# Performance work log

Hardware: AMD Instinct MI355X
Metric: run time of the kernel (lower is better)

Reference implementation:

```python
import jax, jax.numpy as jnp
import numpy as np

B, N, D, NH, T = 4, 1024, 512, 8, 2
H = D // NH  # attention_head_size = 64
NTYPES = 8


def setup_inputs() -> dict:
    key = jax.random.key(0)
    ks = jax.random.split(key, 16)
    w = lambda k, s: jax.random.normal(k, s, jnp.float32) * 0.05
    inp = {
        'node_embedding': jax.random.normal(ks[0], (B, N, D), jnp.float32),
        'question_embedding': jax.random.normal(ks[1], (B, 1, D), jnp.float32),
        'W_fc_w': w(ks[2], (D, 2 * D)),
        'w_dc_w': w(ks[3], (T, 2 * D, D)),
        'dense_w': w(ks[4], (2 * D, 2 * D)),
        'ln_in_g': jnp.ones((2 * D,), jnp.float32), 'ln_in_b': jnp.zeros((2 * D,), jnp.float32),
        'W_qv_w': w(ks[5], (2 * D, D)), 'W_kv_w': w(ks[6], (2 * D, D)), 'W_vv_w': w(ks[7], (2 * D, D)),
        'W_qc_w': w(ks[8], (D, D)), 'W_kc_w': w(ks[9], (D, D)), 'W_vc_w': w(ks[10], (D, D)),
        'ln_q_g': jnp.ones((D,), jnp.float32), 'ln_q_b': jnp.zeros((D,), jnp.float32),
        'ln_k_g': jnp.ones((D,), jnp.float32), 'ln_k_b': jnp.zeros((D,), jnp.float32),
        'ln_v_g': jnp.ones((D,), jnp.float32), 'ln_v_b': jnp.zeros((D,), jnp.float32),
        'W_att': w(ks[11], (1 + NTYPES, 2 * H)),  # row 0 = entity-number, rows 1..8 = number types
        'W_u_w': w(ks[12], (2 * D, D)),
        'ln_out_g': jnp.ones((D,), jnp.float32), 'ln_out_b': jnp.zeros((D,), jnp.float32),
    }
    # masks must be disjoint (assert max(sum of masks) <= 1): partition a categorical
    r = jax.random.randint(ks[13], (B, N, N), 0, NTYPES + 2)
    inp['mask_entity'] = (r == 0).astype(jnp.int32)
    inp['mask_types'] = jnp.stack([(r == k + 1).astype(jnp.int32) for k in range(NTYPES)], 0)
    return inp


def _ln(x, g, b):
    m = jnp.mean(x, -1, keepdims=True)
    v = jnp.mean(jnp.square(x - m), -1, keepdims=True)
    return (x - m) * jax.lax.rsqrt(v + 1e-12) * g + b


def _forward(node_embedding, question_embedding, W_fc_w, w_dc_w, dense_w, ln_in_g, ln_in_b,
             W_qv_w, W_kv_w, W_vv_w, W_qc_w, W_kc_w, W_vc_w,
             ln_q_g, ln_q_b, ln_k_g, ln_k_b, ln_v_g, ln_v_b,
             W_att, W_u_w, ln_out_g, ln_out_b, mask_entity, mask_types):
    node_enc = node_embedding
    # eval mode: dropout is identity
    for t in range(T):
        m_t = jax.nn.elu(question_embedding @ W_fc_w) @ w_dc_w[t]  # [B,1,D]
        ie = jnp.concatenate([node_enc, node_embedding], -1) @ dense_w  # [B,N,2D]
        ie = _ln(ie, ln_in_g, ln_in_b)
        # qd=True: question-directed gating
        xq = _ln((ie @ W_qv_w) * (m_t @ W_qc_w), ln_q_g, ln_q_b)
        xk = _ln((ie @ W_kv_w) * (m_t @ W_kc_w), ln_k_g, ln_k_b)
        xv = _ln((ie @ W_vv_w) * (m_t @ W_vc_w), ln_v_g, ln_v_b)
        split = lambda x: x.reshape(B, N, NH, H).transpose(0, 2, 1, 3)  # [B,H,N,h]
        xq, xk, xv = split(xq), split(xk), split(xv)
        # additive attention W([q_i; k_j]) == q_i.Wq + k_j.Wk : compute rank-1 parts, no NxN concat
        a_src = jnp.einsum('bhnd,md->mbhn', xq, W_att[:, :H])  # [9,B,H,N]
        a_dst = jnp.einsum('bhnd,md->mbhn', xk, W_att[:, H:])
        score = jnp.where(mask_entity[:, None, :, :] > 0,
                          a_src[0][..., :, None] + a_dst[0][..., None, :], 0.0)
        for k in range(NTYPES):
            score = score + jnp.where(mask_types[k][:, None, :, :] > 0,
                                      a_src[k + 1][..., :, None] + a_dst[k + 1][..., None, :], 0.0)
        score = jnp.where(score > 0, score, 0.01 * score)  # F.leaky_relu default slope
        mask_total = (mask_entity + jnp.sum(mask_types, 0))[:, None, :, :].astype(score.dtype)  # [B,1,N,N]
        # allennlp masked_softmax (default branch)
        p = jax.nn.softmax(score * mask_total, axis=-1) * mask_total
        p = p / (jnp.sum(p, -1, keepdims=True) + 1e-13)
        p = jnp.where(mask_total > 0, p, 0.0)
        X = jnp.einsum('bhij,bhjd->bhid', p, xv).transpose(0, 2, 1, 3).reshape(B, N, D)
        node_enc = _ln(jnp.concatenate([node_enc, X], -1) @ W_u_w, ln_out_g, ln_out_b)
    return node_enc


def reference(node_embedding, question_embedding, W_fc_w, w_dc_w, dense_w, ln_in_g, ln_in_b,
              W_qv_w, W_kv_w, W_vv_w, W_qc_w, W_kc_w, W_vc_w,
              ln_q_g, ln_q_b, ln_k_g, ln_k_b, ln_v_g, ln_v_b,
              W_att, W_u_w, ln_out_g, ln_out_b, mask_entity, mask_types):
    return _forward(node_embedding, question_embedding, W_fc_w, w_dc_w, dense_w, ln_in_g, ln_in_b,
                    W_qv_w, W_kv_w, W_vv_w, W_qc_w, W_kc_w, W_vc_w,
                    ln_q_g, ln_q_b, ln_k_g, ln_k_b, ln_v_g, ln_v_b,
                    W_att, W_u_w, ln_out_g, ln_out_b, mask_entity, mask_types)
```

## Files before the change

kernel.cpp:

```cpp
#include <hip/hip_runtime.h>
#include <stdint.h>

typedef unsigned short u16;
typedef short v8s __attribute__((ext_vector_type(8)));
typedef float v4f __attribute__((ext_vector_type(4)));

__device__ __forceinline__ float bf2f(u16 u) {
  union { unsigned int i; float f; } v; v.i = ((unsigned int)u) << 16; return v.f;
}
__device__ __forceinline__ u16 f2bf(float f) {
  union { float f; unsigned int i; } v; v.f = f;
  unsigned int r = v.i + 0x7FFFu + ((v.i >> 16) & 1u);
  return (u16)(r >> 16);
}
__device__ __forceinline__ int probe_f32(const void* p) {
  return ((const u16*)p)[0] != 0x3F80;
}

#define GLOAD16(g, l) __builtin_amdgcn_global_load_lds( \
    (__attribute__((address_space(1))) void*)(g), \
    (__attribute__((address_space(3))) void*)(l), 16, 0, 0)

__launch_bounds__(256)
__global__ void setup_cat(const int4* __restrict__ me,
                          const int4* __restrict__ mt,
                          uchar4* __restrict__ cat) {
  const int base = (blockIdx.x << 10) + threadIdx.x;
  int4 a0 = me[base], a1 = me[base + 256], a2 = me[base + 512], a3 = me[base + 768];
  int c[4][4];
  c[0][0]=a0.x; c[0][1]=a0.y; c[0][2]=a0.z; c[0][3]=a0.w;
  c[1][0]=a1.x; c[1][1]=a1.y; c[1][2]=a1.z; c[1][3]=a1.w;
  c[2][0]=a2.x; c[2][1]=a2.y; c[2][2]=a2.z; c[2][3]=a2.w;
  c[3][0]=a3.x; c[3][1]=a3.y; c[3][2]=a3.z; c[3][3]=a3.w;
  #pragma unroll
  for (int k = 0; k < 8; k++) {
    const int4* mk = mt + ((size_t)k << 20);
    int4 m0 = mk[base], m1 = mk[base + 256], m2 = mk[base + 512], m3 = mk[base + 768];
    const int w = k + 2;
    c[0][0]+=w*m0.x; c[0][1]+=w*m0.y; c[0][2]+=w*m0.z; c[0][3]+=w*m0.w;
    c[1][0]+=w*m1.x; c[1][1]+=w*m1.y; c[1][2]+=w*m1.z; c[1][3]+=w*m1.w;
    c[2][0]+=w*m2.x; c[2][1]+=w*m2.y; c[2][2]+=w*m2.z; c[2][3]+=w*m2.w;
    c[3][0]+=w*m3.x; c[3][1]+=w*m3.y; c[3][2]+=w*m3.z; c[3][3]+=w*m3.w;
  }
  #pragma unroll
  for (int j = 0; j < 4; j++) {
    uchar4 o;
    o.x=(unsigned char)c[j][0]; o.y=(unsigned char)c[j][1];
    o.z=(unsigned char)c[j][2]; o.w=(unsigned char)c[j][3];
    cat[base + j * 256] = o;
  }
}

struct SetupTab {
  const void* csrc[12]; void* cdst[12]; int cn4[12]; int cblk[12];
  const void* tsrc[5];
  u16* dwT; u16* wqkvT;
  const void* probe;
};

__device__ void tr_body(const void* src, u16* dst, int R, int C, int r0, int c0,
                        int f32, u16 (*t)[65]) {
  const int tx = threadIdx.x & 63, ty = threadIdx.x >> 6;
  #pragma unroll
  for (int i = 0; i < 16; i++) {
    int r = (i << 2) + ty;
    size_t off = (size_t)(r0 + r) * C + c0 + tx;
    t[r][tx] = f32 ? f2bf(((const float*)src)[off]) : ((const u16*)src)[off];
  }
  __syncthreads();
  #pragma unroll
  for (int i = 0; i < 16; i++) {
    int c = (i << 2) + ty;
    dst[(size_t)(c0 + c) * R + r0 + tx] = t[tx][c];
  }
}

__launch_bounds__(256)
__global__ void setup_all(SetupTab tab) {
  __shared__ u16 t[64][65];
  const int blk = blockIdx.x, tid = threadIdx.x;
  const int f32 = probe_f32(tab.probe);
  if (blk < 715) {
    int rel = blk, tt = 0;
    while (rel >= tab.cblk[tt]) { rel -= tab.cblk[tt]; tt++; }
    const int n4 = tab.cn4[tt], stride = tab.cblk[tt] << 8;
    const float4* sf = (const float4*)tab.csrc[tt];
    const ushort4* sb = (const ushort4*)tab.csrc[tt];
    ushort4* d = (ushort4*)tab.cdst[tt];
    for (int i = (rel << 8) + tid; i < n4; i += stride) {
      ushort4 o;
      if (f32) { float4 v = sf[i]; o.x=f2bf(v.x); o.y=f2bf(v.y); o.z=f2bf(v.z); o.w=f2bf(v.w); }
      else o = sb[i];
      d[i] = o;
    }
  } else if (blk < 971) {
    const int idx = blk - 715;
    tr_body(tab.tsrc[0], tab.dwT, 1024, 1024, (idx >> 4) << 6, (idx & 15) << 6, f32, t);
  } else {
    const int idx = blk - 971;
    const int tt = idx >> 7, rem = idx & 127;
    tr_body(tab.tsrc[1 + tt], tab.wqkvT + (size_t)tt * 524288,
            1024, 512, (rem >> 3) << 6, (rem & 7) << 6, f32, t);
  }
}

template<int NJ, int MODE>
__launch_bounds__(256, 2)
__global__ void gemm128(const u16* __restrict__ A0, int lda0,
                        const u16* __restrict__ A1, int lda1, int ksplit,
                        const u16* __restrict__ Bm, int ldb,
                        float* __restrict__ Cf, int ldc, int K,
                        const float* __restrict__ gate) {
  constexpr int BN = NJ * 32;
  __shared__ u16 As[128 * 32];
  __shared__ u16 Bs[BN * 32];
  const int tid = threadIdx.x;
  const int wid = tid >> 6, lane = tid & 63;
  const int wr = wid >> 1, wc = wid & 1;
  const int lm = lane & 15, quad = lane >> 4;
  const int m0 = blockIdx.x << 7, n0 = blockIdx.y * BN;

  v4f acc[4][NJ];
  #pragma unroll
  for (int i = 0; i < 4; i++)
    #pragma unroll
    for (int j = 0; j < NJ; j++) acc[i][j] = v4f{0.f,0.f,0.f,0.f};

  const int srow = tid >> 2;
  for (int k0 = 0; k0 < K; k0 += 32) {
    __syncthreads();
    {
      const int kg = k0 + ((tid & 3) << 3);
      const u16* sa0 = (kg < ksplit)
          ? (A0 + (size_t)(m0 + srow) * lda0 + kg)
          : (A1 + (size_t)(m0 + srow) * lda1 + (kg - ksplit));
      GLOAD16(sa0, &As[wid << 9]);
      const u16* sa1 = (kg < ksplit)
          ? (A0 + (size_t)(m0 + 64 + srow) * lda0 + kg)
          : (A1 + (size_t)(m0 + 64 + srow) * lda1 + (kg - ksplit));
      GLOAD16(sa1, &As[2048 + (wid << 9)]);
      GLOAD16(Bm + (size_t)(n0 + srow) * ldb + kg, &Bs[wid << 9]);
      if constexpr (NJ == 4) {
        GLOAD16(Bm + (size_t)(n0 + 64 + srow) * ldb + kg, &Bs[2048 + (wid << 9)]);
      }
    }
    __syncthreads();
    v8s af[4], bfr[NJ];
    #pragma unroll
    for (int i = 0; i < 4; i++)
      af[i] = *(const v8s*)&As[(wr*64 + i*16 + lm)*32 + quad*8];
    #pragma unroll
    for (int j = 0; j < NJ; j++)
      bfr[j] = *(const v8s*)&Bs[(wc*(NJ*16) + j*16 + lm)*32 + quad*8];
    #pragma unroll
    for (int i = 0; i < 4; i++)
      #pragma unroll
      for (int j = 0; j < NJ; j++)
        acc[i][j] = __builtin_amdgcn_mfma_f32_16x16x32_bf16(af[i], bfr[j], acc[i][j], 0, 0, 0);
  }

  #pragma unroll
  for (int i = 0; i < 4; i++) {
    #pragma unroll
    for (int j = 0; j < NJ; j++) {
      int col = n0 + wc*(NJ*16) + j*16 + lm;
      #pragma unroll
      for (int r = 0; r < 4; r++) {
        int row = m0 + wr*64 + i*16 + quad*4 + r;
        float v = acc[i][j][r];
        if (MODE == 0) {
          Cf[(size_t)row * ldc + col] = v;
        } else {
          float g = gate[(((col >> 9) << 2) + (row >> 10)) * 512 + (col & 511)];
          Cf[(size_t)row * ldc + col] = v * g;
        }
      }
    }
  }
}

__launch_bounds__(256)
__global__ void gates_a(const void* __restrict__ q, const void* __restrict__ Wfc,
                        float* __restrict__ t1, const void* probe) {
  __shared__ float qs[2048];
  __shared__ float part[4][4][64];
  const int tid = threadIdx.x;
  const int f32 = probe_f32(probe);
  for (int i = tid; i < 2048; i += 256)
    qs[i] = f32 ? ((const float*)q)[i] : bf2f(((const u16*)q)[i]);
  __syncthreads();
  const int col = (blockIdx.x << 6) + (tid & 63);
  const int kq = tid >> 6;
  float a0 = 0, a1 = 0, a2 = 0, a3 = 0;
  if (f32) {
    const float* W = (const float*)Wfc;
    for (int kk = 0; kk < 128; kk++) {
      int k = kq * 128 + kk;
      float w = W[(size_t)k * 1024 + col];
      a0 += qs[k]*w; a1 += qs[512+k]*w; a2 += qs[1024+k]*w; a3 += qs[1536+k]*w;
    }
  } else {
    const u16* W = (const u16*)Wfc;
    for (int kk = 0; kk < 128; kk++) {
      int k = kq * 128 + kk;
      float w = bf2f(W[(size_t)k * 1024 + col]);
      a0 += qs[k]*w; a1 += qs[512+k]*w; a2 += qs[1024+k]*w; a3 += qs[1536+k]*w;
    }
  }
  part[kq][0][tid&63]=a0; part[kq][1][tid&63]=a1;
  part[kq][2][tid&63]=a2; part[kq][3][tid&63]=a3;
  __syncthreads();
  const int b = tid >> 6, c = tid & 63;
  float s = part[0][b][c]+part[1][b][c]+part[2][b][c]+part[3][b][c];
  s = s > 0.f ? s : __expf(s) - 1.0f;
  t1[(b << 10) + (blockIdx.x << 6) + c] = s;
}

__launch_bounds__(256)
__global__ void gates_b(const float* __restrict__ t1, const void* __restrict__ wdc,
                        float* __restrict__ mt, const void* probe) {
  __shared__ float ts[4096];
  __shared__ float part[4][4][64];
  const int tid = threadIdx.x;
  const int f32 = probe_f32(probe);
  for (int i = tid; i < 4096; i += 256) ts[i] = t1[i];
  __syncthreads();
  const int t = blockIdx.y;
  const int col = (blockIdx.x << 6) + (tid & 63);
  const int kq = tid >> 6;
  float a0 = 0, a1 = 0, a2 = 0, a3 = 0;
  if (f32) {
    const float* W = (const float*)wdc;
    for (int kk = 0; kk < 256; kk++) {
      int k = kq * 256 + kk;
      float w = W[((size_t)(t << 10) + k) * 512 + col];
      a0 += ts[k]*w; a1 += ts[1024+k]*w; a2 += ts[2048+k]*w; a3 += ts[3072+k]*w;
    }
  } else {
    const u16* W = (const u16*)wdc;
    for (int kk = 0; kk < 256; kk++) {
      int k = kq * 256 + kk;
      float w = bf2f(W[((size_t)(t << 10) + k) * 512 + col]);
      a0 += ts[k]*w; a1 += ts[1024+k]*w; a2 += ts[2048+k]*w; a3 += ts[3072+k]*w;
    }
  }
  part[kq][0][tid&63]=a0; part[kq][1][tid&63]=a1;
  part[kq][2][tid&63]=a2; part[kq][3][tid&63]=a3;
  __syncthreads();
  const int b = tid >> 6, c = tid & 63;
  float s = part[0][b][c]+part[1][b][c]+part[2][b][c]+part[3][b][c];
  mt[((t * 4 + b) << 9) + (blockIdx.x << 6) + c] = s;
}

__launch_bounds__(256)
__global__ void gates_c(const float* __restrict__ mt,
                        const void* __restrict__ Wqc, const void* __restrict__ Wkc,
                        const void* __restrict__ Wvc, float* __restrict__ gates,
                        const void* probe) {
  __shared__ float ms[2048];
  __shared__ float part[4][4][64];
  const int tid = threadIdx.x;
  const int f32 = probe_f32(probe);
  const int s_ = blockIdx.y, t = blockIdx.z;
  for (int i = tid; i < 2048; i += 256) ms[i] = mt[(t << 11) + i];
  __syncthreads();
  const void* W = (s_ == 0) ? Wqc : ((s_ == 1) ? Wkc : Wvc);
  const int col = (blockIdx.x << 6) + (tid & 63);
  const int kq = tid >> 6;
  float a0 = 0, a1 = 0, a2 = 0, a3 = 0;
  if (f32) {
    const float* Wf = (const float*)W;
    for (int kk = 0; kk < 128; kk++) {
      int k = kq * 128 + kk;
      float w = Wf[(size_t)k * 512 + col];
      a0 += ms[k]*w; a1 += ms[512+k]*w; a2 += ms[1024+k]*w; a3 += ms[1536+k]*w;
    }
  } else {
    const u16* Wb = (const u16*)W;
    for (int kk = 0; kk < 128; kk++) {
      int k = kq * 128 + kk;
      float w = bf2f(Wb[(size_t)k * 512 + col]);
      a0 += ms[k]*w; a1 += ms[512+k]*w; a2 += ms[1024+k]*w; a3 += ms[1536+k]*w;
    }
  }
  part[kq][0][tid&63]=a0; part[kq][1][tid&63]=a1;
  part[kq][2][tid&63]=a2; part[kq][3][tid&63]=a3;
  __syncthreads();
  const int b = tid >> 6, c = tid & 63;
  float s = part[0][b][c]+part[1][b][c]+part[2][b][c]+part[3][b][c];
  gates[(((t * 3 + s_) * 4 + b) << 9) + (blockIdx.x << 6) + c] = s;
}

template<int NE>
__launch_bounds__(256)
__global__ void ln_rows(const float* __restrict__ src, int sstride, int ssegoff,
                        void* __restrict__ dst, int dstride, int dsegoff,
                        int finalout, const void* probe,
                        const u16* __restrict__ g0, const u16* __restrict__ b0,
                        const u16* __restrict__ g1, const u16* __restrict__ b1,
                        const u16* __restrict__ g2, const u16* __restrict__ b2) {
  constexpr int W = NE * 256;
  const int row = blockIdx.x, seg = blockIdx.y;
  const u16* g  = (seg == 0) ? g0 : ((seg == 1) ? g1 : g2);
  const u16* bb = (seg == 0) ? b0 : ((seg == 1) ? b1 : b2);
  const float* x = src + (size_t)row * sstride + (size_t)seg * ssegoff;
  const size_t dbase = (size_t)row * dstride + (size_t)seg * dsegoff;
  const int f32out = finalout ? probe_f32(probe) : 0;
  const int tid = threadIdx.x;
  const int wid = tid >> 6, lane = tid & 63;
  __shared__ float red[4];
  float v[NE];
  float s = 0.f;
  #pragma unroll
  for (int i = 0; i < NE; i++) { v[i] = x[tid + (i << 8)]; s += v[i]; }
  #pragma unroll
  for (int off = 32; off; off >>= 1) s += __shfl_xor(s, off, 64);
  if (lane == 0) red[wid] = s;
  __syncthreads();
  float mean = (red[0]+red[1]+red[2]+red[3]) * (1.0f / W);
  float q = 0.f;
  #pragma unroll
  for (int i = 0; i < NE; i++) { float dd = v[i] - mean; q += dd * dd; }
  __syncthreads();
  #pragma unroll
  for (int off = 32; off; off >>= 1) q += __shfl_xor(q, off, 64);
  if (lane == 0) red[wid] = q;
  __syncthreads();
  float var = (red[0]+red[1]+red[2]+red[3]) * (1.0f / W);
  float rs = rsqrtf(var + 1e-12f);
  #pragma unroll
  for (int i = 0; i < NE; i++) {
    int c = tid + (i << 8);
    float y = (v[i] - mean) * rs * bf2f(g[c]) + bf2f(bb[c]);
    if (f32out) ((float*)dst)[dbase + c] = y;
    else        ((u16*)dst)[dbase + c] = f2bf(y);
  }
}

__launch_bounds__(256)
__global__ void proj_and_xvt(const u16* __restrict__ xqkv, const u16* __restrict__ Watt,
                             float* __restrict__ asrc, float* __restrict__ adst,
                             u16* __restrict__ xvT) {
  __shared__ char shraw[8320];
  const int blk = blockIdx.x, tid = threadIdx.x;
  if (blk >= 1024) {
    const int idx = blk - 1024;
    const int z = idx >> 7, rem = idx & 127;
    tr_body(xqkv + 2ull*4096*512 + (size_t)z * 524288, xvT + (size_t)z * 524288,
            1024, 512, (rem >> 3) << 6, (rem & 7) << 6, 0, (u16(*)[65])shraw);
    return;
  }
  float (*w)[128] = (float(*)[128])shraw;
  for (int i = tid; i < 9 * 128; i += 256) w[i / 128][i % 128] = bf2f(Watt[i]);
  __syncthreads();
  const int wid = tid >> 6, lane = tid & 63;
  const int row = blk * 4 + wid;
  const int b = row >> 10, n = row & 1023;
  const u16* xq = xqkv;
  const u16* xk = xqkv + 4096ull*512;
  v8s q8 = *(const v8s*)&xq[(size_t)row * 512 + lane * 8];
  v8s k8 = *(const v8s*)&xk[(size_t)row * 512 + lane * 8];
  float qf[8], kf[8];
  #pragma unroll
  for (int j = 0; j < 8; j++) { qf[j] = bf2f((u16)q8[j]); kf[j] = bf2f((u16)k8[j]); }
  const int h = lane >> 3, lh = lane & 7;
  #pragma unroll
  for (int m = 0; m < 9; m++) {
    float ps = 0.f, pd = 0.f;
    #pragma unroll
    for (int j = 0; j < 8; j++) {
      ps += qf[j] * w[m][lh * 8 + j];
      pd += kf[j] * w[m][64 + lh * 8 + j];
    }
    #pragma unroll
    for (int off = 1; off < 8; off <<= 1) {
      ps += __shfl_xor(ps, off, 64);
      pd += __shfl_xor(pd, off, 64);
    }
    if (lh == 0) {
      size_t base = (size_t)(b * 8 + h) * 9216 + n * 9 + m;
      asrc[base] = ps;
      adst[base] = pd;
    }
  }
}

__launch_bounds__(256)
__global__ void attn_pv(const unsigned char* __restrict__ cat,
                        const float* __restrict__ asrc,
                        const float* __restrict__ adst,
                        const u16* __restrict__ xvT,
                        u16* __restrict__ xcat) {
  const int bh = blockIdx.y;
  const int b = bh >> 3, h = bh & 7;
  const int i0 = blockIdx.x << 6;
  __shared__ __align__(16) float adst_s[9216];
  __shared__ __align__(16) u16 P_lds[16 * 1032];
  __shared__ float asrc_s[576];
  __shared__ float inv_s[16];
  const int tid = threadIdx.x;
  const float* ad = adst + (size_t)bh * 9216;
  for (int i = tid; i < 9216; i += 256) adst_s[i] = ad[i];
  const float* as = asrc + (size_t)bh * 9216 + (size_t)i0 * 9;
  for (int i = tid; i < 576; i += 256) asrc_s[i] = as[i];
  __syncthreads();
  const int wid = tid >> 6, lane = tid & 63;
  const int lm = lane & 15, quad = lane >> 4;

  for (int ph = 0; ph < 4; ph++) {
    if (ph) __syncthreads();
    #pragma unroll
    for (int rr = 0; rr < 4; rr++) {
      const int lr = wid * 4 + rr;
      const int r  = ph * 16 + lr;
      const u16* crow = (const u16*)(cat + (((size_t)(b << 10) + i0 + r) << 10));
      float sum = 0.f;
      #pragma unroll
      for (int s = 0; s < 8; s++) {
        const int j0 = s * 128 + lane * 2;
        unsigned int cc2 = crow[s * 64 + lane];
        float z0 = 0.f, z1 = 0.f;
        int c0 = cc2 & 255, c1 = (cc2 >> 8) & 255;
        if (c0) {
          float sc = asrc_s[r * 9 + c0 - 1] + adst_s[j0 * 9 + c0 - 1];
          z0 = __expf(sc > 0.f ? sc : 0.01f * sc);
        }
        if (c1) {
          float sc = asrc_s[r * 9 + c1 - 1] + adst_s[(j0 + 1) * 9 + c1 - 1];
          z1 = __expf(sc > 0.f ? sc : 0.01f * sc);
        }
        sum += z0 + z1;
        unsigned int pk = (unsigned int)f2bf(z0) | ((unsigned int)f2bf(z1) << 16);
        ((unsigned int*)P_lds)[(lr * 1032 + j0) >> 1] = pk;
      }
      #pragma unroll
      for (int off = 32; off; off >>= 1) sum += __shfl_xor(sum, off, 64);
      if (lane == 0) inv_s[lr] = 1.0f / (sum + 1e-13f);
    }
    __syncthreads();
    v4f acc = v4f{0.f, 0.f, 0.f, 0.f};
    const u16* xvc = xvT + ((size_t)(bh << 6) + (wid * 16 + lm)) * 1024;
    for (int c = 0; c < 32; c++) {
      v8s a = *(const v8s*)&P_lds[lm * 1032 + c * 32 + quad * 8];
      v8s bf = *(const v8s*)&xvc[c * 32 + quad * 8];
      acc = __builtin_amdgcn_mfma_f32_16x16x32_bf16(a, bf, acc, 0, 0, 0);
    }
    #pragma unroll
    for (int r = 0; r < 4; r++) {
      const int lrow = quad * 4 + r;
      const int grow = i0 + ph * 16 + lrow;
      float v = acc[r] * inv_s[lrow];
      xcat[(((size_t)(b << 10) + grow) << 9) + (h << 6) + wid * 16 + lm] = f2bf(v);
    }
  }
}

extern "C" void kernel_launch(void* const* d_in, const int* in_sizes, int n_in,
                              void* d_out, int out_size, void* d_ws, size_t ws_size,
                              hipStream_t stream) {
  char* wptr = (char*)d_ws;
  auto alloc = [&](size_t bytes) {
    char* p = wptr; wptr += (bytes + 255) & ~(size_t)255; return p;
  };
  uint8_t* cat   = (uint8_t*)alloc(4ull << 20);
  u16* dwT       = (u16*)alloc(1024ull*1024*2);
  u16* wqkvT     = (u16*)alloc(2048ull*1024*2);
  u16* wuT       = wqkvT + 1536*1024;
  float* gates   = (float*)alloc(2ull*3*4*512*4);
  float* t1buf   = (float*)alloc(4096ull*4);
  float* mtbuf   = (float*)alloc(4096ull*4);
  u16* c_node    = (u16*)alloc(2097152ull*2);
  u16* c_small   = (u16*)alloc(16384ull*2);
  float* ie_pre  = (float*)alloc(4096ull*1024*4);
  float* qkv_pre = (float*)alloc(4096ull*1536*4);
  u16* ie        = (u16*)alloc(4096ull*1024*2);
  u16* xqkv      = (u16*)alloc(3ull*4096*512*2);
  float* asrc    = (float*)alloc(32ull*9216*4);
  float* adst    = (float*)alloc(32ull*9216*4);
  u16* xvT       = (u16*)alloc(32ull*64*1024*2);
  u16* xcat      = (u16*)alloc(4096ull*512*2);
  float* u_pre   = (float*)alloc(4096ull*512*4);
  u16* node_enc  = (u16*)alloc(4096ull*512*2);

  const void* probe = d_in[5];

  static const int sidx[11] = {5, 6, 13, 14, 15, 16, 17, 18, 19, 21, 22};
  static const int ssz[11]  = {1024, 1024, 512, 512, 512, 512, 512, 512, 1152, 512, 512};
  u16* sp[11]; int off = 0;
  for (int i = 0; i < 11; i++) { sp[i] = c_small + off; off += (ssz[i] + 127) & ~127; }
  const u16 *c_lin_g = sp[0], *c_lin_b = sp[1];
  const u16 *c_lq_g = sp[2], *c_lq_b = sp[3];
  const u16 *c_lk_g = sp[4], *c_lk_b = sp[5];
  const u16 *c_lv_g = sp[6], *c_lv_b = sp[7];
  const u16 *c_Watt = sp[8];
  const u16 *c_lo_g = sp[9], *c_lo_b = sp[10];

  SetupTab tab;
  tab.csrc[0] = d_in[0]; tab.cdst[0] = c_node; tab.cn4[0] = 2097152/4; tab.cblk[0] = 704;
  for (int i = 0; i < 11; i++) {
    tab.csrc[1+i] = d_in[sidx[i]]; tab.cdst[1+i] = sp[i];
    tab.cn4[1+i] = ssz[i] / 4; tab.cblk[1+i] = 1;
  }
  tab.tsrc[0] = d_in[4];
  tab.tsrc[1] = d_in[7];
  tab.tsrc[2] = d_in[8];
  tab.tsrc[3] = d_in[9];
  tab.tsrc[4] = d_in[20];
  tab.dwT = dwT; tab.wqkvT = wqkvT;
  tab.probe = probe;

  setup_cat<<<1024, 256, 0, stream>>>((const int4*)d_in[23], (const int4*)d_in[24],
                                      (uchar4*)cat);
  setup_all<<<1483, 256, 0, stream>>>(tab);
  gates_a<<<16, 256, 0, stream>>>(d_in[1], d_in[2], t1buf, probe);
  gates_b<<<dim3(8,2), 256, 0, stream>>>(t1buf, d_in[3], mtbuf, probe);
  gates_c<<<dim3(8,3,2), 256, 0, stream>>>(mtbuf, d_in[10], d_in[11], d_in[12],
                                           gates, probe);

  const u16* ne_cur = c_node;
  for (int t = 0; t < 2; ++t) {
    gemm128<4,0><<<dim3(32,8), 256, 0, stream>>>(
        ne_cur, 512, c_node, 512, 512, dwT, 1024, ie_pre, 1024, 1024, nullptr);
    ln_rows<4><<<dim3(4096,1), 256, 0, stream>>>(
        ie_pre, 1024, 0, ie, 1024, 0, 0, probe,
        c_lin_g, c_lin_b, c_lin_g, c_lin_b, c_lin_g, c_lin_b);
    gemm128<4,1><<<dim3(32,12), 256, 0, stream>>>(
        ie, 1024, ie, 1024, 1024, wqkvT, 1024, qkv_pre, 1536, 1024, gates + t*6144);
    ln_rows<2><<<dim3(4096,3), 256, 0, stream>>>(
        qkv_pre, 1536, 512, xqkv, 512, 4096*512, 0, probe,
        c_lq_g, c_lq_b, c_lk_g, c_lk_b, c_lv_g, c_lv_b);
    proj_and_xvt<<<1536, 256, 0, stream>>>(xqkv, c_Watt, asrc, adst, xvT);
    attn_pv<<<dim3(16,32), 256, 0, stream>>>(cat, asrc, adst, xvT, xcat);
    gemm128<2,0><<<dim3(32,8), 256, 0, stream>>>(
        ne_cur, 512, xcat, 512, 512, wuT, 1024, u_pre, 512, 1024, nullptr);
    void* dst = (t == 1) ? d_out : (void*)node_enc;
    ln_rows<2><<<dim3(4096,1), 256, 0, stream>>>(
        u_pre, 512, 0, dst, 512, 0, (t == 1) ? 1 : 0, probe,
        c_lo_g, c_lo_b, c_lo_g, c_lo_b, c_lo_g, c_lo_b);
    ne_cur = node_enc;
  }
  (void)in_sizes; (void)n_in; (void)out_size; (void)ws_size;
}
```

Baseline: 668.1 us.

## Pipeline GEMM K-loop with four-stage LDS ring and async prefetch

Replaces the single-buffered GEMM, which loaded and then waited on each K-slice, with a templated kernel. It keeps a four-slot LDS ring and issues global-to-LDS loads two slices ahead, using explicit vmcnt waits so memory latency overlaps with MFMA work. The output-projection GEMM is also retiled to 64x128 blocks with a 1x4 warp layout, giving more blocks along M. The cost is four times the LDS per block, which may limit occupancy, and more complex wait-count bookkeeping.

```diff
diff --git a/kernel.cpp b/kernel.cpp
--- a/kernel.cpp
+++ b/kernel.cpp
@@ -104,21 +104,45 @@
   }
 }
 
-template<int NJ, int MODE>
+template<int BM, int NJ, int MODE>
 __launch_bounds__(256, 2)
-__global__ void gemm128(const u16* __restrict__ A0, int lda0,
-                        const u16* __restrict__ A1, int lda1, int ksplit,
-                        const u16* __restrict__ Bm, int ldb,
-                        float* __restrict__ Cf, int ldc, int K,
-                        const float* __restrict__ gate) {
-  constexpr int BN = NJ * 32;
-  __shared__ u16 As[128 * 32];
-  __shared__ u16 Bs[BN * 32];
+__global__ void gemm_p(const u16* __restrict__ A0, int lda0,
+                       const u16* __restrict__ A1, int lda1, int ksplit,
+                       const u16* __restrict__ Bm, int ldb,
+                       float* __restrict__ Cf, int ldc, int K,
+                       const float* __restrict__ gate) {
+  constexpr int WR = (BM == 128) ? 2 : 1;
+  constexpr int WC = 4 / WR;
+  constexpr int BN = WC * NJ * 16;
+  constexpr int RA = BM / 64, RB = BN / 64, R = RA + RB;
+  constexpr int TSZ = (BM + BN) * 32;
+  __shared__ u16 lds[4 * TSZ];
   const int tid = threadIdx.x;
   const int wid = tid >> 6, lane = tid & 63;
-  const int wr = wid >> 1, wc = wid & 1;
+  const int wr = (WR == 2) ? (wid >> 1) : 0;
+  const int wc = (WR == 2) ? (wid & 1) : wid;
   const int lm = lane & 15, quad = lane >> 4;
-  const int m0 = blockIdx.x << 7, n0 = blockIdx.y * BN;
+  const int m0 = blockIdx.x * BM, n0 = blockIdx.y * BN;
+  const int srow = tid >> 2;
+  const int kcol = (tid & 3) << 3;
+
+  auto stage = [&](int buf, int k0) {
+    u16* Ad = lds + buf * TSZ;
+    u16* Bd = Ad + BM * 32;
+    const int kg = k0 + kcol;
+    #pragma unroll
+    for (int p = 0; p < RA; p++) {
+      const int row = m0 + (p << 6) + srow;
+      const u16* s = (kg < ksplit) ? (A0 + (size_t)row * lda0 + kg)
+                                   : (A1 + (size_t)row * lda1 + (kg - ksplit));
+      GLOAD16(s, &Ad[(p << 11) + (wid << 9)]);
+    }
+    #pragma unroll
+    for (int p = 0; p < RB; p++) {
+      GLOAD16(Bm + (size_t)(n0 + (p << 6) + srow) * ldb + kg,
+              &Bd[(p << 11) + (wid << 9)]);
+    }
+  };
 
   v4f acc[4][NJ];
   #pragma unroll
@@ -126,32 +150,31 @@
     #pragma unroll
     for (int j = 0; j < NJ; j++) acc[i][j] = v4f{0.f,0.f,0.f,0.f};
 
-  const int srow = tid >> 2;
-  for (int k0 = 0; k0 < K; k0 += 32) {
+  const int S = K >> 5;
+  stage(0, 0);
+  int issued = 1;
+  if (S > 1) { stage(1, 32); issued = 2; }
+
+  for (int s = 0; s < S; s++) {
+    if (issued < S) { stage(issued & 3, issued << 5); issued++; }
+    const int fly = issued - s;
+    if (fly >= 3) {
+      asm volatile("s_waitcnt vmcnt(%0)" :: "n"(2 * R) : "memory");
+    } else if (fly == 2) {
+      asm volatile("s_waitcnt vmcnt(%0)" :: "n"(R) : "memory");
+    } else {
+      asm volatile("s_waitcnt vmcnt(0)" ::: "memory");
+    }
     __syncthreads();
-    {
-      const int kg = k0 + ((tid & 3) << 3);
-      const u16* sa0 = (kg < ksplit)
-          ? (A0 + (size_t)(m0 + srow) * lda0 + kg)
-          : (A1 + (size_t)(m0 + srow) * lda1 + (kg - ksplit));
-      GLOAD16(sa0, &As[wid << 9]);
-      const u16* sa1 = (kg < ksplit)
-          ? (A0 + (size_t)(m0 + 64 + srow) * lda0 + kg)
-          : (A1 + (size_t)(m0 + 64 + srow) * lda1 + (kg - ksplit));
-      GLOAD16(sa1, &As[2048 + (wid << 9)]);
-      GLOAD16(Bm + (size_t)(n0 + srow) * ldb + kg, &Bs[wid << 9]);
-      if constexpr (NJ == 4) {
-        GLOAD16(Bm + (size_t)(n0 + 64 + srow) * ldb + kg, &Bs[2048 + (wid << 9)]);
-      }
-    }
-    __syncthreads();
+    const u16* Ab = lds + (s & 3) * TSZ;
+    const u16* Bb = Ab + BM * 32;
     v8s af[4], bfr[NJ];
     #pragma unroll
     for (int i = 0; i < 4; i++)
-      af[i] = *(const v8s*)&As[(wr*64 + i*16 + lm)*32 + quad*8];
+      af[i] = *(const v8s*)&Ab[(wr*64 + i*16 + lm)*32 + quad*8];
     #pragma unroll
     for (int j = 0; j < NJ; j++)
-      bfr[j] = *(const v8s*)&Bs[(wc*(NJ*16) + j*16 + lm)*32 + quad*8];
+      bfr[j] = *(const v8s*)&Bb[(wc*(NJ*16) + j*16 + lm)*32 + quad*8];
     #pragma unroll
     for (int i = 0; i < 4; i++)
       #pragma unroll
@@ -519,19 +542,19 @@
 
   const u16* ne_cur = c_node;
   for (int t = 0; t < 2; ++t) {
-    gemm128<4,0><<<dim3(32,8), 256, 0, stream>>>(
+    gemm_p<128,4,0><<<dim3(32,8), 256, 0, stream>>>(
         ne_cur, 512, c_node, 512, 512, dwT, 1024, ie_pre, 1024, 1024, nullptr);
     ln_rows<4><<<dim3(4096,1), 256, 0, stream>>>(
         ie_pre, 1024, 0, ie, 1024, 0, 0, probe,
         c_lin_g, c_lin_b, c_lin_g, c_lin_b, c_lin_g, c_lin_b);
-    gemm128<4,1><<<dim3(32,12), 256, 0, stream>>>(
+    gemm_p<128,4,1><<<dim3(32,12), 256, 0, stream>>>(
         ie, 1024, ie, 1024, 1024, wqkvT, 1024, qkv_pre, 1536, 1024, gates + t*6144);
     ln_rows<2><<<dim3(4096,3), 256, 0, stream>>>(
         qkv_pre, 1536, 512, xqkv, 512, 4096*512, 0, probe,
         c_lq_g, c_lq_b, c_lk_g, c_lk_b, c_lv_g, c_lv_b);
     proj_and_xvt<<<1536, 256, 0, stream>>>(xqkv, c_Watt, asrc, adst, xvT);
     attn_pv<<<dim3(16,32), 256, 0, stream>>>(cat, asrc, adst, xvT, xcat);
-    gemm128<2,0><<<dim3(32,8), 256, 0, stream>>>(
+    gemm_p<64,2,0><<<dim3(64,4), 256, 0, stream>>>(
         ne_cur, 512, xcat, 512, 512, wuT, 1024, u_pre, 512, 1024, nullptr);
     void* dst = (t == 1) ? d_out : (void*)node_enc;
     ln_rows<2><<<dim3(4096,1), 256, 0, stream>>>(
```

Result: no change. 661.2 us (-1.0%).
